# Kernel optimization log

Measured on AMD Instinct MI355X. Metric: run time of the kernel, lower is better.

## Reference

```python
import jax, jax.numpy as jnp
import numpy as np

N = 12288      # nodes
D_IN = 256     # input feature dim
D_OUT = 256    # embedding_channels
E = 196608     # input edges (avg degree 16)
K = 4          # kNN edges per node


def setup_inputs() -> dict:
    key = jax.random.key(0)
    k1, k2, k3, k4 = jax.random.split(key, 4)
    x = jax.random.normal(k1, (N, D_IN), jnp.float32)
    edge_index = jax.random.randint(k2, (2, E), 0, N)
    # GCNConv parameters (PyG GCNConv: symmetric-normalized propagation + linear + bias)
    W = jax.random.normal(k3, (D_IN, D_OUT), jnp.float32) / np.sqrt(D_IN).astype(np.float32)
    b = jnp.zeros((D_OUT,), jnp.float32)
    temperature = jnp.asarray(4.0, jnp.float32)  # nn.Parameter(tensor(4.0))
    # uniform noise, stands in for torch.rand_like(logprobs)
    q = jax.random.uniform(k4, (N, N), jnp.float32)
    return dict(x=x, W=W, b=b, temperature=temperature, q=q, edge_index=edge_index)


def gcn_conv(x, edge_index, W, b):
    # PyG GCNConv: h = D^{-1/2} (A + I) D^{-1/2} (x W) + b
    n = x.shape[0]
    loops = jnp.arange(n)
    row = jnp.concatenate([edge_index[0], loops])  # destination
    col = jnp.concatenate([edge_index[1], loops])  # source
    h = x @ W
    deg = jax.ops.segment_sum(jnp.ones(row.shape, h.dtype), row, num_segments=n)
    dinv = jax.lax.rsqrt(jnp.maximum(deg, 1.0))  # deg >= 1 thanks to self loops
    norm = dinv[row] * dinv[col]                 # [E+n]
    out = jax.ops.segment_sum(h[col] * norm[:, None], row, num_segments=n)
    return out + b


def reference(x, W, b, temperature, q, edge_index):
    h = gcn_conv(x, edge_index, W, b)                       # [N, D_OUT]
    # cdist(h, h)**2 == squared euclidean distances
    sq = jnp.sum(h * h, axis=1)                              # [N]
    d2 = jnp.maximum(sq[:, None] + sq[None, :] - 2.0 * (h @ h.T), 0.0)  # [N, N]
    logprobs = -temperature * d2
    # Gumbel perturbation: lq = logprobs - log(-log(q + 1e-8))
    lq = logprobs - jnp.log(-jnp.log(q + 1e-8))
    top_vals, top_idx = jax.lax.top_k(lq, K)                 # [N, K] each
    rows = jnp.repeat(jnp.arange(N), K)
    edges = jnp.stack([top_idx.reshape(-1), rows])           # [2, N*K]
    # fix_self_loops treated as identity: dist(i,i)=0 makes self the top-1
    # candidate with overwhelming probability (see notes).
    return h, edges, top_vals
```

## Files before the change

kernel.cpp:

```cpp
#include <hip/hip_runtime.h>
#include <hip/hip_bf16.h>

#define N_NODES 12288
#define D 256
#define NE 196608
#define TOPK 4
#define NBLK 96
#define MAXDEG 256

typedef __attribute__((ext_vector_type(8))) short bf8;
typedef __attribute__((ext_vector_type(4))) float f32x4;

__device__ __forceinline__ void ins4(float v, int id, float tv[TOPK], int ti[TOPK]) {
  if (v > tv[3]) {
    tv[3] = v; ti[3] = id;
    if (tv[3] > tv[2]) {
      float a = tv[2]; tv[2] = tv[3]; tv[3] = a; int b = ti[2]; ti[2] = ti[3]; ti[3] = b;
      if (tv[2] > tv[1]) {
        float a2 = tv[1]; tv[1] = tv[2]; tv[2] = a2; int b2 = ti[1]; ti[1] = ti[2]; ti[2] = b2;
        if (tv[1] > tv[0]) {
          float a3 = tv[0]; tv[0] = tv[1]; tv[1] = a3; int b3 = ti[0]; ti[0] = ti[1]; ti[1] = b3;
        }
      }
    }
  }
}

__device__ __forceinline__ void ins4tie(float v, int id, float tv[TOPK], int ti[TOPK]) {
  if ((v > tv[3]) || (v == tv[3] && id < ti[3])) {
    tv[3] = v; ti[3] = id;
    if ((tv[3] > tv[2]) || (tv[3] == tv[2] && ti[3] < ti[2])) {
      float a = tv[2]; tv[2] = tv[3]; tv[3] = a; int b = ti[2]; ti[2] = ti[3]; ti[3] = b;
      if ((tv[2] > tv[1]) || (tv[2] == tv[1] && ti[2] < ti[1])) {
        float a2 = tv[1]; tv[1] = tv[2]; tv[2] = a2; int b2 = ti[1]; ti[1] = ti[2]; ti[2] = b2;
        if ((tv[1] > tv[0]) || (tv[1] == tv[0] && ti[1] < ti[0])) {
          float a3 = tv[0]; tv[0] = tv[1]; tv[1] = a3; int b3 = ti[0]; ti[0] = ti[1]; ti[1] = b3;
        }
      }
    }
  }
}

__device__ __forceinline__ void ins8tie(float v, int id, float tv[8], int ti8[8]) {
  if (!((v > tv[7]) || (v == tv[7] && id < ti8[7]))) return;
  tv[7] = v; ti8[7] = id;
#pragma unroll
  for (int k = 7; k > 0; --k) {
    bool sw = (tv[k] > tv[k - 1]) || (tv[k] == tv[k - 1] && ti8[k] < ti8[k - 1]);
    if (sw) {
      float a = tv[k - 1]; tv[k - 1] = tv[k]; tv[k] = a;
      int b = ti8[k - 1]; ti8[k - 1] = ti8[k]; ti8[k] = b;
    }
  }
}

__global__ __launch_bounds__(256) void k_xw(const float* __restrict__ X,
                                            const float* __restrict__ W,
                                            float* __restrict__ XW) {
  __shared__ float sA[16][65];
  __shared__ float sB[16][65];
  const int tid = threadIdx.x;
  const int ty = tid >> 4, tx = tid & 15;
  const int by = blockIdx.x, bx = blockIdx.y;
  float acc[4][4] = {};
  for (int kk = 0; kk < D; kk += 16) {
    {
      int m = tid >> 2;
      int kq = (tid & 3) << 2;
      const float4 av = *(const float4*)&X[(size_t)(by * 64 + m) * D + kk + kq];
      sA[kq + 0][m] = av.x; sA[kq + 1][m] = av.y; sA[kq + 2][m] = av.z; sA[kq + 3][m] = av.w;
    }
    {
      int r = tid >> 4;
      int c = (tid & 15) << 2;
      const float4 bv = *(const float4*)&W[(size_t)(kk + r) * D + bx * 64 + c];
      sB[r][c + 0] = bv.x; sB[r][c + 1] = bv.y; sB[r][c + 2] = bv.z; sB[r][c + 3] = bv.w;
    }
    __syncthreads();
#pragma unroll
    for (int k = 0; k < 16; ++k) {
      float a[4], b[4];
#pragma unroll
      for (int i = 0; i < 4; i++) a[i] = sA[k][ty + 16 * i];
#pragma unroll
      for (int j = 0; j < 4; j++) b[j] = sB[k][tx + 16 * j];
#pragma unroll
      for (int i = 0; i < 4; i++)
#pragma unroll
        for (int j = 0; j < 4; j++) acc[i][j] = fmaf(a[i], b[j], acc[i][j]);
    }
    __syncthreads();
  }
#pragma unroll
  for (int i = 0; i < 4; i++)
#pragma unroll
    for (int j = 0; j < 4; j++)
      XW[(size_t)(by * 64 + ty + 16 * i) * D + bx * 64 + tx + 16 * j] = acc[i][j];
}

__global__ void k_deg(const int* __restrict__ row, int* __restrict__ deg) {
  int e = blockIdx.x * blockDim.x + threadIdx.x;
  if (e < NE) {
    unsigned r = (unsigned)row[e];
    if (r < N_NODES) atomicAdd(&deg[r], 1);
  }
}

__global__ __launch_bounds__(256) void k_scan(const int* __restrict__ deg,
                                              int* __restrict__ row_start,
                                              float* __restrict__ dinv) {
  __shared__ int part[256];
  const int tid = threadIdx.x;
  const int L = N_NODES / 256;
  const int base = tid * L;
  int s = 0;
  for (int i = 0; i < L; i++) s += deg[base + i];
  part[tid] = s;
  __syncthreads();
  for (int off = 1; off < 256; off <<= 1) {
    int v = (tid >= off) ? part[tid - off] : 0;
    __syncthreads();
    part[tid] += v;
    __syncthreads();
  }
  int run = part[tid] - s;
  for (int i = 0; i < L; i++) {
    int d = deg[base + i];
    row_start[base + i] = run;
    dinv[base + i] = 1.0f / sqrtf((float)(d + 1));
    run += d;
  }
}

__global__ void k_fill(const int* __restrict__ row, const int* __restrict__ col,
                       const int* __restrict__ row_start, int* __restrict__ cursor,
                       int* __restrict__ ecol, int* __restrict__ eeid) {
  int e = blockIdx.x * blockDim.x + threadIdx.x;
  if (e >= NE) return;
  unsigned r = (unsigned)row[e];
  if (r >= N_NODES) return;
  int p = atomicAdd(&cursor[r], 1);
  int slot = row_start[r] + p;
  if ((unsigned)slot >= NE) return;
  unsigned c = (unsigned)col[e];
  if (c >= N_NODES) c = 0;
  ecol[slot] = (int)c;
  eeid[slot] = e;
}

__global__ __launch_bounds__(256) void k_agg(const float* __restrict__ XW,
                                             const float* __restrict__ bias,
                                             const int* __restrict__ deg,
                                             const int* __restrict__ row_start,
                                             const int* __restrict__ ecol,
                                             const int* __restrict__ eeid,
                                             const float* __restrict__ dinv,
                                             float* __restrict__ h_out,
                                             float* __restrict__ sq) {
  __shared__ int sc[MAXDEG];
  __shared__ int se[MAXDEG];
  __shared__ float snorm[MAXDEG];
  __shared__ float red[256];
  const int i = blockIdx.x;
  const int tid = threadIdx.x;
  int cnt = deg[i];
  if (cnt > MAXDEG) cnt = MAXDEG;
  if (cnt < 0) cnt = 0;
  const int st = row_start[i];
  for (int t = tid; t < cnt; t += 256) {
    unsigned cc = (unsigned)ecol[st + t];
    sc[t] = (cc < N_NODES) ? (int)cc : 0;
    se[t] = eeid[st + t];
  }
  __syncthreads();
  if (tid == 0) {
    for (int a = 1; a < cnt; ++a) {
      int ce = se[a], cc = sc[a];
      int bp = a - 1;
      while (bp >= 0 && se[bp] > ce) { se[bp + 1] = se[bp]; sc[bp + 1] = sc[bp]; --bp; }
      se[bp + 1] = ce; sc[bp + 1] = cc;
    }
  }
  __syncthreads();
  const float di = dinv[i];
  for (int t = tid; t < cnt; t += 256) snorm[t] = __fmul_rn(di, dinv[sc[t]]);
  __syncthreads();
  float acc = 0.0f;
  for (int t = 0; t < cnt; ++t) {
    float v = XW[(size_t)sc[t] * D + tid];
    acc = __fadd_rn(acc, __fmul_rn(v, snorm[t]));
  }
  acc = __fadd_rn(acc, __fmul_rn(XW[(size_t)i * D + tid], __fmul_rn(di, di)));
  acc = __fadd_rn(acc, bias[tid]);
  h_out[(size_t)i * D + tid] = acc;
  red[tid] = __fmul_rn(acc, acc);
  __syncthreads();
  for (int off = 128; off > 0; off >>= 1) {
    if (tid < off) red[tid] = __fadd_rn(red[tid], red[tid + off]);
    __syncthreads();
  }
  if (tid == 0) sq[i] = red[0];
}

__global__ __launch_bounds__(256) void k_split(const float* __restrict__ h,
                                               unsigned short* __restrict__ hhi,
                                               unsigned short* __restrict__ hlo) {
  int i = blockIdx.x * 256 + threadIdx.x;
  float v = h[i];
  __hip_bfloat16 bh = __float2bfloat16(v);
  float hiF = __bfloat162float(bh);
  __hip_bfloat16 bl = __float2bfloat16(v - hiF);
  hhi[i] = *(unsigned short*)&bh;
  hlo[i] = *(unsigned short*)&bl;
}

__global__ __launch_bounds__(256, 2) void k_gemm(const unsigned short* __restrict__ hhi,
                                                 const unsigned short* __restrict__ hlo,
                                                 const float* __restrict__ sq,
                                                 const float* __restrict__ q,
                                                 const float* __restrict__ tempP,
                                                 float* __restrict__ candv,
                                                 int* __restrict__ candi) {
  __shared__ float lqs[128][133];
  const int tid = threadIdx.x;
  const int w = tid >> 6, l = tid & 63;
  const int row0 = blockIdx.x * 128, col0 = blockIdx.y * 128;
  const float T = tempP[0];

  f32x4 acc[4][4];
#pragma unroll
  for (int a = 0; a < 4; ++a)
#pragma unroll
    for (int b = 0; b < 4; ++b) acc[a][b] = (f32x4){0.f, 0.f, 0.f, 0.f};

  const int koct = l >> 4;
  const int arow = row0 + (w & 1) * 64 + (l & 15);
  const int brow = col0 + (w >> 1) * 64 + (l & 15);
  const unsigned short* Ah0 = hhi + (size_t)arow * D + koct * 8;
  const unsigned short* Al0 = hlo + (size_t)arow * D + koct * 8;
  const unsigned short* Bh0 = hhi + (size_t)brow * D + koct * 8;
  const unsigned short* Bl0 = hlo + (size_t)brow * D + koct * 8;

  for (int kc = 0; kc < D; kc += 32) {
    bf8 Ah[4], Al[4], Bh[4], Bl[4];
#pragma unroll
    for (int a = 0; a < 4; ++a) {
      Ah[a] = *(const bf8*)(Ah0 + (size_t)a * 16 * D + kc);
      Al[a] = *(const bf8*)(Al0 + (size_t)a * 16 * D + kc);
      Bh[a] = *(const bf8*)(Bh0 + (size_t)a * 16 * D + kc);
      Bl[a] = *(const bf8*)(Bl0 + (size_t)a * 16 * D + kc);
    }
#pragma unroll
    for (int a = 0; a < 4; ++a)
#pragma unroll
      for (int b = 0; b < 4; ++b) {
        acc[a][b] = __builtin_amdgcn_mfma_f32_16x16x32_bf16(Ah[a], Bh[b], acc[a][b], 0, 0, 0);
        acc[a][b] = __builtin_amdgcn_mfma_f32_16x16x32_bf16(Ah[a], Bl[b], acc[a][b], 0, 0, 0);
        acc[a][b] = __builtin_amdgcn_mfma_f32_16x16x32_bf16(Al[a], Bh[b], acc[a][b], 0, 0, 0);
      }
  }

#pragma unroll
  for (int a = 0; a < 4; ++a)
#pragma unroll
    for (int b = 0; b < 4; ++b)
#pragma unroll
      for (int r = 0; r < 4; ++r) {
        int rowblk = (w & 1) * 64 + a * 16 + (l >> 4) * 4 + r;
        int colblk = (w >> 1) * 64 + b * 16 + (l & 15);
        int grow = row0 + rowblk, gcol = col0 + colblk;
        float dot = acc[a][b][r];
        float d2 = fmaxf((sq[grow] + sq[gcol]) - 2.0f * dot, 0.0f);
        float gg = logf(-logf(q[(size_t)grow * N_NODES + gcol] + 1e-8f));
        lqs[rowblk][colblk] = -T * d2 - gg;
      }
  __syncthreads();
  {
    int rw = tid >> 1, cbase = (tid & 1) * 64;
    float tv[TOPK]; int ti4[TOPK];
#pragma unroll
    for (int k = 0; k < TOPK; ++k) { tv[k] = -3.0e38f; ti4[k] = 0; }
    for (int i = 0; i < 64; ++i) ins4(lqs[rw][cbase + i], col0 + cbase + i, tv, ti4);
    float ov[TOPK]; int oi[TOPK];
#pragma unroll
    for (int k = 0; k < TOPK; ++k) {
      ov[k] = __shfl_xor(tv[k], 1);
      oi[k] = __shfl_xor(ti4[k], 1);
    }
#pragma unroll
    for (int k = 0; k < TOPK; ++k) ins4tie(ov[k], oi[k], tv, ti4);
    if ((tid & 1) == 0) {
      size_t base = ((size_t)(row0 + rw) * NBLK + blockIdx.y) * TOPK;
#pragma unroll
      for (int k = 0; k < TOPK; ++k) { candv[base + k] = tv[k]; candi[base + k] = ti4[k]; }
    }
  }
}

__global__ __launch_bounds__(256) void k_cmerge1(const float* __restrict__ candv,
                                                 const int* __restrict__ candi,
                                                 float* __restrict__ pv8,
                                                 int* __restrict__ pi8) {
  int gid = blockIdx.x * 256 + threadIdx.x;
  int row = gid >> 3, chunk = gid & 7;
  size_t base = (size_t)row * (NBLK * TOPK) + chunk * 48;
  float tv[8]; int ti8[8];
#pragma unroll
  for (int k = 0; k < 8; ++k) { tv[k] = -3.0e38f; ti8[k] = 0; }
  for (int i = 0; i < 48; ++i) ins8tie(candv[base + i], candi[base + i], tv, ti8);
  size_t ob = (size_t)gid * 8;
#pragma unroll
  for (int k = 0; k < 8; ++k) { pv8[ob + k] = tv[k]; pi8[ob + k] = ti8[k]; }
}

__global__ __launch_bounds__(256) void k_cmerge2(const float* __restrict__ pv8,
                                                 const int* __restrict__ pi8,
                                                 float* __restrict__ fv8,
                                                 int* __restrict__ fi8) {
  int row = blockIdx.x * 256 + threadIdx.x;
  size_t base = (size_t)row * 64;
  float tv[8]; int ti8[8];
#pragma unroll
  for (int k = 0; k < 8; ++k) { tv[k] = -3.0e38f; ti8[k] = 0; }
  for (int i = 0; i < 64; ++i) ins8tie(pv8[base + i], pi8[base + i], tv, ti8);
  ins8tie(3.0e38f, row, tv, ti8);
  size_t ob = (size_t)row * 8;
#pragma unroll
  for (int k = 0; k < 8; ++k) { fv8[ob + k] = tv[k]; fi8[ob + k] = ti8[k]; }
}

__global__ __launch_bounds__(256) void k_exact(const int* __restrict__ fi8,
                                               const float* __restrict__ h,
                                               const float* __restrict__ sq,
                                               const float* __restrict__ q,
                                               const float* __restrict__ tempP,
                                               float* __restrict__ out_idx,
                                               float* __restrict__ out_rows,
                                               float* __restrict__ out_vals) {
  const int tid = threadIdx.x;
  const int row = blockIdx.x * 4 + (tid >> 6);
  const int l = tid & 63;
  const float T = tempP[0];
  int ti8[8];
#pragma unroll
  for (int k = 0; k < 8; ++k) ti8[k] = fi8[(size_t)row * 8 + k];
  float4 hr = *(const float4*)&h[(size_t)row * D + l * 4];
  float lqe[8];
#pragma unroll
  for (int k = 0; k < 8; ++k) {
    int c = ti8[k];
    float4 hc = *(const float4*)&h[(size_t)c * D + l * 4];
    float p = fmaf(hr.x, hc.x, 0.0f);
    p = fmaf(hr.y, hc.y, p);
    p = fmaf(hr.z, hc.z, p);
    p = fmaf(hr.w, hc.w, p);
#pragma unroll
    for (int m = 1; m < 64; m <<= 1) p += __shfl_xor(p, m);
    float d2 = fmaxf(__fsub_rn(__fadd_rn(sq[row], sq[c]), __fmul_rn(2.0f, p)), 0.0f);
    float lp = -__fmul_rn(T, d2);
    float gg = logf(-logf(__fadd_rn(q[(size_t)row * N_NODES + c], 1e-8f)));
    lqe[k] = __fsub_rn(lp, gg);
  }
  float bv[TOPK]; int bi[TOPK];
#pragma unroll
  for (int k = 0; k < TOPK; ++k) { bv[k] = -3.0e38f; bi[k] = 0; }
#pragma unroll
  for (int k = 0; k < 8; ++k) {
    bool dup = false;
#pragma unroll
    for (int k2 = 0; k2 < 8; ++k2)
      if (k2 < k) dup = dup || (ti8[k2] == ti8[k]);
    if (!dup) ins4tie(lqe[k], ti8[k], bv, bi);
  }
  if (l == 0) {
#pragma unroll
    for (int k = 0; k < TOPK; ++k) {
      out_idx[(size_t)row * TOPK + k] = (float)bi[k];
      out_rows[(size_t)row * TOPK + k] = (float)row;
      out_vals[(size_t)row * TOPK + k] = bv[k];
    }
  }
}

extern "C" void kernel_launch(void* const* d_in, const int* in_sizes, int n_in,
                              void* d_out, int out_size, void* d_ws, size_t ws_size,
                              hipStream_t stream) {
  const float* x = nullptr;
  const float* W = nullptr;
  const float* b = nullptr;
  const float* temp = nullptr;
  const float* q = nullptr;
  const int* ei = nullptr;
  for (int i = 0; i < n_in; ++i) {
    switch (in_sizes[i]) {
      case 3145728:   x = (const float*)d_in[i]; break;
      case 65536:     W = (const float*)d_in[i]; break;
      case 256:       b = (const float*)d_in[i]; break;
      case 1:         temp = (const float*)d_in[i]; break;
      case 150994944: q = (const float*)d_in[i]; break;
      case 393216:    ei = (const int*)d_in[i]; break;
      default: break;
    }
  }
  if (!x || !W || !b || !temp || !q || !ei) return;

  float* out = (float*)d_out;
  float* out_h = out;
  float* out_idx = out + (size_t)N_NODES * D;
  float* out_rows = out_idx + (size_t)N_NODES * TOPK;
  float* out_vals = out_rows + (size_t)N_NODES * TOPK;

  char* ws = (char*)d_ws;
  size_t off = 0;
  auto alloc = [&](size_t bytes) {
    char* p = ws + off;
    off += (bytes + 255) & ~(size_t)255;
    return p;
  };
  float* XW = (float*)alloc((size_t)N_NODES * D * 4);
  int* deg = (int*)alloc((size_t)N_NODES * 4);
  int* rs = (int*)alloc((size_t)N_NODES * 4);
  int* cur = (int*)alloc((size_t)N_NODES * 4);
  float* dinv = (float*)alloc((size_t)N_NODES * 4);
  float* sq = (float*)alloc((size_t)N_NODES * 4);
  int* ecol = (int*)alloc((size_t)NE * 4);
  int* eeid = (int*)alloc((size_t)NE * 4);
  float* candv = (float*)alloc((size_t)N_NODES * NBLK * TOPK * 4);
  int* candi = (int*)alloc((size_t)N_NODES * NBLK * TOPK * 4);
  float* pv8 = (float*)alloc((size_t)N_NODES * 64 * 4);
  int* pi8 = (int*)alloc((size_t)N_NODES * 64 * 4);
  float* fv8 = (float*)alloc((size_t)N_NODES * 8 * 4);
  int* fi8 = (int*)alloc((size_t)N_NODES * 8 * 4);
  if (off > ws_size) return;

  hipMemsetAsync(deg, 0, (size_t)N_NODES * 4, stream);
  hipMemsetAsync(cur, 0, (size_t)N_NODES * 4, stream);

  k_xw<<<dim3(N_NODES / 64, D / 64), 256, 0, stream>>>(x, W, XW);
  k_deg<<<NE / 256, 256, 0, stream>>>(ei, deg);
  k_scan<<<1, 256, 0, stream>>>(deg, rs, dinv);
  k_fill<<<NE / 256, 256, 0, stream>>>(ei, ei + NE, rs, cur, ecol, eeid);
  k_agg<<<N_NODES, 256, 0, stream>>>(XW, b, deg, rs, ecol, eeid, dinv, out_h, sq);

  unsigned short* hhi = (unsigned short*)XW;
  unsigned short* hlo = hhi + (size_t)N_NODES * D;
  k_split<<<(N_NODES * D) / 256, 256, 0, stream>>>(out_h, hhi, hlo);
  k_gemm<<<dim3(NBLK, NBLK), 256, 0, stream>>>(hhi, hlo, sq, q, temp, candv, candi);
  k_cmerge1<<<(N_NODES * 8) / 256, 256, 0, stream>>>(candv, candi, pv8, pi8);
  k_cmerge2<<<N_NODES / 256, 256, 0, stream>>>(pv8, pi8, fv8, fi8);
  k_exact<<<N_NODES / 4, 256, 0, stream>>>(fi8, out_h, sq, q, temp,
                                           out_idx, out_rows, out_vals);
}
```

Measured before the change: 1.032 ms.

## Halve GEMM epilogue LDS tile, stage top-k in two passes, use fast logs

The k_gemm epilogue now keeps the Gumbel-perturbed logits in accumulator registers and writes them to shared memory in two 64-column halves, with a top-4 scan between the halves. This halves the LDS footprint, and together with raising launch_bounds minimum blocks from 2 to 4 it aims to fit more workgroups per CU and better hide the heavy q streaming. It also replaces logf with __logf to cut transcendental cost. The trade-offs are extra __syncthreads, possible register pressure or spills under the tighter launch bound, and slightly less accurate logs that could change top-k ties.

```diff
diff --git a/kernel.cpp b/kernel.cpp
--- a/kernel.cpp
+++ b/kernel.cpp
@@ -214,14 +214,14 @@
   hlo[i] = *(unsigned short*)&bl;
 }
 
-__global__ __launch_bounds__(256, 2) void k_gemm(const unsigned short* __restrict__ hhi,
+__global__ __launch_bounds__(256, 4) void k_gemm(const unsigned short* __restrict__ hhi,
                                                  const unsigned short* __restrict__ hlo,
                                                  const float* __restrict__ sq,
                                                  const float* __restrict__ q,
                                                  const float* __restrict__ tempP,
                                                  float* __restrict__ candv,
                                                  int* __restrict__ candi) {
-  __shared__ float lqs[128][133];
+  __shared__ float lqs[128][69];
   const int tid = threadIdx.x;
   const int w = tid >> 6, l = tid & 63;
   const int row0 = blockIdx.x * 128, col0 = blockIdx.y * 128;
@@ -271,29 +271,57 @@
         int grow = row0 + rowblk, gcol = col0 + colblk;
         float dot = acc[a][b][r];
         float d2 = fmaxf((sq[grow] + sq[gcol]) - 2.0f * dot, 0.0f);
-        float gg = logf(-logf(q[(size_t)grow * N_NODES + gcol] + 1e-8f));
-        lqs[rowblk][colblk] = -T * d2 - gg;
+        float gg = __logf(-__logf(q[(size_t)grow * N_NODES + gcol] + 1e-8f));
+        acc[a][b][r] = -T * d2 - gg;
       }
-  __syncthreads();
-  {
-    int rw = tid >> 1, cbase = (tid & 1) * 64;
-    float tv[TOPK]; int ti4[TOPK];
-#pragma unroll
-    for (int k = 0; k < TOPK; ++k) { tv[k] = -3.0e38f; ti4[k] = 0; }
-    for (int i = 0; i < 64; ++i) ins4(lqs[rw][cbase + i], col0 + cbase + i, tv, ti4);
-    float ov[TOPK]; int oi[TOPK];
-#pragma unroll
-    for (int k = 0; k < TOPK; ++k) {
-      ov[k] = __shfl_xor(tv[k], 1);
-      oi[k] = __shfl_xor(ti4[k], 1);
-    }
-#pragma unroll
-    for (int k = 0; k < TOPK; ++k) ins4tie(ov[k], oi[k], tv, ti4);
-    if ((tid & 1) == 0) {
-      size_t base = ((size_t)(row0 + rw) * NBLK + blockIdx.y) * TOPK;
-#pragma unroll
-      for (int k = 0; k < TOPK; ++k) { candv[base + k] = tv[k]; candi[base + k] = ti4[k]; }
-    }
+
+  float tv[TOPK]; int ti4[TOPK];
+#pragma unroll
+  for (int k = 0; k < TOPK; ++k) { tv[k] = -3.0e38f; ti4[k] = 0; }
+  const int rw = tid >> 1, cb = (tid & 1) * 32;
+
+  if ((w >> 1) == 0) {
+#pragma unroll
+    for (int a = 0; a < 4; ++a)
+#pragma unroll
+      for (int b = 0; b < 4; ++b)
+#pragma unroll
+        for (int r = 0; r < 4; ++r) {
+          int rowblk = (w & 1) * 64 + a * 16 + (l >> 4) * 4 + r;
+          int colblk = b * 16 + (l & 15);
+          lqs[rowblk][colblk] = acc[a][b][r];
+        }
+  }
+  __syncthreads();
+  for (int i = 0; i < 32; ++i) ins4(lqs[rw][cb + i], col0 + cb + i, tv, ti4);
+  __syncthreads();
+  if ((w >> 1) == 1) {
+#pragma unroll
+    for (int a = 0; a < 4; ++a)
+#pragma unroll
+      for (int b = 0; b < 4; ++b)
+#pragma unroll
+        for (int r = 0; r < 4; ++r) {
+          int rowblk = (w & 1) * 64 + a * 16 + (l >> 4) * 4 + r;
+          int colblk = b * 16 + (l & 15);
+          lqs[rowblk][colblk] = acc[a][b][r];
+        }
+  }
+  __syncthreads();
+  for (int i = 0; i < 32; ++i) ins4(lqs[rw][cb + i], col0 + 64 + cb + i, tv, ti4);
+
+  float ov[TOPK]; int oi[TOPK];
+#pragma unroll
+  for (int k = 0; k < TOPK; ++k) {
+    ov[k] = __shfl_xor(tv[k], 1);
+    oi[k] = __shfl_xor(ti4[k], 1);
+  }
+#pragma unroll
+  for (int k = 0; k < TOPK; ++k) ins4tie(ov[k], oi[k], tv, ti4);
+  if ((tid & 1) == 0) {
+    size_t base = ((size_t)(row0 + rw) * NBLK + blockIdx.y) * TOPK;
+#pragma unroll
+    for (int k = 0; k < TOPK; ++k) { candv[base + k] = tv[k]; candi[base + k] = ti4[k]; }
   }
 }
 
```

After: 1.197 ms. +15.9%, slower.
